# Performance work log

Measured on AMD Instinct MI355X. Metric: run time of the kernel, lower is better.

## Reference

```python
import jax, jax.numpy as jnp
import numpy as np
from jax import lax

B, P, T = 64, 16, 256
I, H, O = 256, 512, 5
V = 50000


def setup_inputs() -> dict:
    key = jax.random.key(0)
    ks = jax.random.split(key, 16)
    xav = lambda k, shape: jax.random.normal(k, shape, dtype=jnp.float32) * np.sqrt(2.0 / (shape[-2] + shape[-1]))
    inp = {
        "x": jax.random.randint(ks[0], (B, P, T), 0, V),
        "emb": jax.random.normal(ks[1], (V, I), dtype=jnp.float32) * 0.02,
        "W_forget_x": xav(ks[2], (P, I, H)),
        "W_forget_h": xav(ks[3], (H, H)),
        "b_forget": jnp.zeros((H,), jnp.float32),
        "W_ic_x": xav(ks[4], (P, I, H)),
        "W_ic_h": xav(ks[5], (H, H)),
        "b_ic": jnp.zeros((H,), jnp.float32),
        "W_in_x": xav(ks[6], (P, I, H)),
        "W_in_h": xav(ks[7], (H, H)),
        "b_in": jnp.zeros((H,), jnp.float32),
        "W_o_x": xav(ks[8], (P, I, H)),
        "W_o_h": xav(ks[9], (H, H)),
        "b_o": jnp.zeros((H,), jnp.float32),
        "W_lin": xav(ks[10], (H, O)),
        "b_lin": jnp.zeros((O,), jnp.float32),
    }
    return inp


def reference(x, emb, W_forget_x, W_forget_h, b_forget, W_ic_x, W_ic_h, b_ic,
              W_in_x, W_in_h, b_in, W_o_x, W_o_h, b_o, W_lin, b_lin):
    # padding_idx=0: row 0 of the embedding table is zero
    tbl = emb.at[0].set(0.0)
    xe = tbl[x]  # [B, P, T, I]
    # x-side gate pre-activations, summed over POS tags, hoisted out of the recurrence
    pre_f = jnp.einsum('bpti,pih->tbh', xe, W_forget_x) + b_forget  # [T, B, H]
    pre_i = jnp.einsum('bpti,pih->tbh', xe, W_ic_x) + b_ic
    pre_g = jnp.einsum('bpti,pih->tbh', xe, W_in_x) + b_in
    pre_o = jnp.einsum('bpti,pih->tbh', xe, W_o_x) + b_o

    def step(carry, pres):
        h, c = carry
        pf, pi, pg, po = pres
        f = jax.nn.sigmoid(pf + h @ W_forget_h)
        i = jax.nn.sigmoid(pi + h @ W_ic_h)
        g = jnp.tanh(pg + h @ W_in_h)
        o = jax.nn.sigmoid(po + h @ W_o_h)
        c = f * c + i * g
        h = o * jnp.tanh(c)
        return (h, c), None

    bs = x.shape[0]
    h0 = jnp.zeros((bs, W_forget_h.shape[0]), jnp.float32)
    c0 = jnp.zeros_like(h0)
    (h_t, c_t), _ = lax.scan(step, (h0, c0), (pre_f, pre_i, pre_g, pre_o))
    out = h_t @ W_lin + b_lin  # [B, O]
    return out, h_t, c_t
```

## Files before the change

### kernel.cpp

```cpp
#include <hip/hip_runtime.h>
#include <stdint.h>

#define DEVI __device__ __forceinline__
typedef unsigned long long ull;

typedef __bf16 bf16x8 __attribute__((ext_vector_type(8)));
typedef float floatx4 __attribute__((ext_vector_type(4)));

DEVI uint16_t f2bf(float f) {
  union { float f; uint32_t u; } c; c.f = f;
  uint32_t u = c.u;
  return (uint16_t)((u + 0x7fffu + ((u >> 16) & 1u)) >> 16);
}
DEVI float bf2f(uint16_t h) {
  union { uint32_t u; float f; } c; c.u = ((uint32_t)h) << 16;
  return c.f;
}
DEVI void load_lds_16(const void* g, void* l) {
  __builtin_amdgcn_global_load_lds(
      (const __attribute__((address_space(1))) void*)g,
      (__attribute__((address_space(3))) void*)l, 16, 0, 0);
}
DEVI float sigm(float x) { return 1.f / (1.f + __expf(-x)); }
DEVI float tanh_s(float x) {
  float xc = fminf(fmaxf(x, -15.f), 15.f);
  float e = __expf(2.f * xc);
  return (e - 1.f) / (e + 1.f);
}

static constexpr size_t OFF_EMB   = 0;
static constexpr size_t OFF_TS01  = 0;
static constexpr size_t OFF_WXT   = 25600000;
static constexpr size_t OFF_WHT   = OFF_WXT + 16777216;
static constexpr size_t OFF_BIAS  = OFF_WHT + 2097152;
static constexpr size_t OFF_PRE   = OFF_BIAS + 8192;
static constexpr size_t OFF_HF    = OFF_PRE + 67108864 + 4096;
static constexpr size_t OFF_CF    = OFF_HF + 131072;

__global__ __launch_bounds__(256) void k_emb_cvt(const float* __restrict__ emb,
                                                 uint16_t* __restrict__ dst) {
  size_t tid = (size_t)blockIdx.x * 256 + threadIdx.x;
  size_t e = tid * 8;
  int v = (int)(e >> 8);
  const float4* s = (const float4*)(emb + e);
  float4 f0 = s[0], f1 = s[1];
  if (v == 0) { f0 = make_float4(0.f, 0.f, 0.f, 0.f); f1 = f0; }
  uint32_t w0 = f2bf(f0.x) | ((uint32_t)f2bf(f0.y) << 16);
  uint32_t w1 = f2bf(f0.z) | ((uint32_t)f2bf(f0.w) << 16);
  uint32_t w2 = f2bf(f1.x) | ((uint32_t)f2bf(f1.y) << 16);
  uint32_t w3 = f2bf(f1.z) | ((uint32_t)f2bf(f1.w) << 16);
  *(uint4*)(dst + e) = make_uint4(w0, w1, w2, w3);
}

__global__ __launch_bounds__(256) void k_wt(const float* __restrict__ w0, const float* __restrict__ w1,
                                            const float* __restrict__ w2, const float* __restrict__ w3,
                                            int K, uint16_t* __restrict__ dst) {
  __shared__ float tile[64 * 64];
  int k0 = blockIdx.x * 64;
  int n0 = blockIdx.y * 64;
  int h0 = blockIdx.y * 16;
  int g = threadIdx.x >> 6, di = threadIdx.x & 63;
  const float* w = (g == 0) ? w0 : (g == 1) ? w1 : (g == 2) ? w2 : w3;
  const float4* src = (const float4*)(w + (size_t)(k0 + di) * 512 + h0);
  float4 a = src[0], b = src[1], c = src[2], d = src[3];
  float vals[16] = {a.x, a.y, a.z, a.w, b.x, b.y, b.z, b.w,
                    c.x, c.y, c.z, c.w, d.x, d.y, d.z, d.w};
#pragma unroll
  for (int dh = 0; dh < 16; ++dh) tile[(dh * 4 + g) * 64 + di] = vals[dh];
  __syncthreads();
  int nl = threadIdx.x >> 2, ch = threadIdx.x & 3;
  uint32_t wb[8];
#pragma unroll
  for (int j = 0; j < 8; ++j) {
    float lo = tile[nl * 64 + ch * 16 + j * 2];
    float hi = tile[nl * 64 + ch * 16 + j * 2 + 1];
    wb[j] = f2bf(lo) | ((uint32_t)f2bf(hi) << 16);
  }
  uint4* dp = (uint4*)(dst + (size_t)(n0 + nl) * K + k0 + ch * 16);
  dp[0] = make_uint4(wb[0], wb[1], wb[2], wb[3]);
  dp[1] = make_uint4(wb[4], wb[5], wb[6], wb[7]);
}

__global__ __launch_bounds__(256) void k_bias(const float* __restrict__ b0, const float* __restrict__ b1,
                                              const float* __restrict__ b2, const float* __restrict__ b3,
                                              float* __restrict__ dst) {
  int n = blockIdx.x * 256 + threadIdx.x;
  int h = n >> 2, g = n & 3;
  const float* b = (g == 0) ? b0 : (g == 1) ? b1 : (g == 2) ? b2 : b3;
  dst[n] = b[h];
}

__global__ __launch_bounds__(256) void k_gemm(const uint16_t* __restrict__ embbf,
                                              const int* __restrict__ x,
                                              const uint16_t* __restrict__ wxt,
                                              uint16_t* __restrict__ pre) {
  __shared__ uint16_t As[128 * 64];
  __shared__ uint16_t Bs[128 * 64];
  const int tid = threadIdx.x;
  const int wv = tid >> 6, ln = tid & 63;
  const int wm = wv >> 1, wn = wv & 1;
  const int M0 = blockIdx.x * 128, N0 = blockIdx.y * 128;
  const int srow = ln >> 3, schunk = ln & 7;

  const int* xrow[4];
  const uint16_t* bbase[4];
  uint16_t* ldsA[4];
  uint16_t* ldsB[4];
#pragma unroll
  for (int j = 0; j < 4; ++j) {
    int r = j * 32 + wv * 8 + srow;
    int m = M0 + r;
    int t = m >> 6, b = m & 63;
    xrow[j] = x + b * 4096 + t;
    bbase[j] = wxt + (size_t)(N0 + r) * 4096 + schunk * 8;
    ldsA[j] = As + (j * 32 + wv * 8) * 64;
    ldsB[j] = Bs + (j * 32 + wv * 8) * 64;
  }

  const int q = ln >> 4, l16 = ln & 15;
  int aoff[4], boff[4];
#pragma unroll
  for (int mt = 0; mt < 4; ++mt) aoff[mt] = (wm * 64 + mt * 16 + l16) * 64 + q * 8;
#pragma unroll
  for (int nt = 0; nt < 4; ++nt) boff[nt] = (wn * 64 + nt * 16 + l16) * 64 + q * 8;

  floatx4 acc[4][4] = {};

  for (int p = 0; p < 16; ++p) {
    const uint16_t* abase[4];
#pragma unroll
    for (int j = 0; j < 4; ++j) {
      int idx = xrow[j][p << 8];
      abase[j] = embbf + (size_t)idx * 256 + schunk * 8;
    }
#pragma unroll 1
    for (int ki = 0; ki < 4; ++ki) {
      __syncthreads();
#pragma unroll
      for (int j = 0; j < 4; ++j) load_lds_16(abase[j] + ki * 64, ldsA[j]);
#pragma unroll
      for (int j = 0; j < 4; ++j) load_lds_16(bbase[j] + p * 256 + ki * 64, ldsB[j]);
      __syncthreads();
#pragma unroll
      for (int kk = 0; kk < 2; ++kk) {
        bf16x8 a[4];
#pragma unroll
        for (int mt = 0; mt < 4; ++mt) a[mt] = *(const bf16x8*)(As + aoff[mt] + kk * 32);
#pragma unroll
        for (int nt = 0; nt < 4; ++nt) {
          bf16x8 bv = *(const bf16x8*)(Bs + boff[nt] + kk * 32);
#pragma unroll
          for (int mt = 0; mt < 4; ++mt)
            acc[mt][nt] = __builtin_amdgcn_mfma_f32_16x16x32_bf16(a[mt], bv, acc[mt][nt], 0, 0, 0);
        }
      }
    }
  }

#pragma unroll
  for (int mt = 0; mt < 4; ++mt) {
    int mg = M0 + wm * 64 + mt * 16 + q * 4;
#pragma unroll
    for (int nt = 0; nt < 4; ++nt) {
      int ng = N0 + wn * 64 + nt * 16 + l16;
#pragma unroll
      for (int r = 0; r < 4; ++r)
        pre[(size_t)(mg + r) * 2048 + ng] = f2bf(acc[mt][nt][r]);
    }
  }
}

__global__ __launch_bounds__(256) void k_rec(const uint16_t* pre,
                                             char* preb,
                                             char* scratch,
                                             const uint16_t* __restrict__ wht,
                                             const float* __restrict__ bias,
                                             float* __restrict__ hfin,
                                             float* __restrict__ cfin) {
  __shared__ uint16_t Ahs[2][16 * 544];
  __shared__ uint16_t pres[2][16 * 128];
  __shared__ float gates[16 * 132];

  const int tid = threadIdx.x;
  const int wv = tid >> 6, ln = tid & 63;
  const int q = ln >> 4, l16 = ln & 15;
  const int bg = blockIdx.x >> 4, cg = blockIdx.x & 15;
  const int N0 = cg * 128;

  bf16x8 Bfrag[16][2];
#pragma unroll
  for (int kc = 0; kc < 16; ++kc)
#pragma unroll
    for (int nt = 0; nt < 2; ++nt) {
      int n = N0 + wv * 32 + nt * 16 + l16;
      Bfrag[kc][nt] = *(const bf16x8*)(wht + (size_t)n * 512 + kc * 32 + q * 8);
    }
  float breg[2];
#pragma unroll
  for (int nt = 0; nt < 2; ++nt) breg[nt] = bias[N0 + wv * 32 + nt * 16 + l16];

  const int prow = wv * 4 + (ln >> 4);
  const int pj = ln & 15;
  const int erow = ln >> 2;
  const int es = ln & 3;
  float creg[2] = {0.f, 0.f};

  for (int i = tid; i < 4352; i += 256) ((uint32_t*)Ahs[0])[i] = 0;
  {
    const uint16_t* g = pre + (size_t)(bg * 16 + wv * 4 + (ln >> 4)) * 2048 + N0 + (ln & 15) * 8;
    load_lds_16(g, (uint16_t*)pres[0] + wv * 512);
  }

  for (int t = 0; t < 256; ++t) {
    if (t > 0) {
      const char* sb = (t - 1 < 2) ? scratch + (size_t)(t - 1) * 262144
                                   : preb + (size_t)(t - 3) * 262144;
      const ull* pp = (const ull*)(sb + (size_t)bg * 65536 + prow * 2048 + pj * 8);
      const uint32_t want = (uint32_t)t;
      ull v[16];
      bool ok = false;
      while (!ok) {
        ok = true;
#pragma unroll
        for (int j = 0; j < 16; ++j)
          v[j] = __hip_atomic_load(pp + j * 16, __ATOMIC_RELAXED, __HIP_MEMORY_SCOPE_AGENT);
#pragma unroll
        for (int j = 0; j < 16; ++j)
          ok = ok && ((uint32_t)(v[j] >> 32) == want);
        if (!ok) __builtin_amdgcn_s_sleep(1);
      }
      uint16_t* dr = Ahs[t & 1] + prow * 544;
#pragma unroll
      for (int j = 0; j < 16; ++j)
        *(uint32_t*)(dr + 2 * pj + 32 * j) = (uint32_t)v[j];
    }
    __syncthreads();

    const uint16_t* Ab = Ahs[t & 1];
    floatx4 a0[2] = {}, a1[2] = {};
#pragma unroll
    for (int kc = 0; kc < 8; ++kc) {
      bf16x8 a = *(const bf16x8*)(Ab + l16 * 544 + kc * 32 + q * 8);
#pragma unroll
      for (int nt = 0; nt < 2; ++nt)
        a0[nt] = __builtin_amdgcn_mfma_f32_16x16x32_bf16(a, Bfrag[kc][nt], a0[nt], 0, 0, 0);
    }
#pragma unroll
    for (int kc = 8; kc < 16; ++kc) {
      bf16x8 a = *(const bf16x8*)(Ab + l16 * 544 + kc * 32 + q * 8);
#pragma unroll
      for (int nt = 0; nt < 2; ++nt)
        a1[nt] = __builtin_amdgcn_mfma_f32_16x16x32_bf16(a, Bfrag[kc][nt], a1[nt], 0, 0, 0);
    }

    const uint16_t* pcur = (const uint16_t*)pres[t & 1];
#pragma unroll
    for (int nt = 0; nt < 2; ++nt) {
      int n_l = wv * 32 + nt * 16 + l16;
      floatx4 s = a0[nt] + a1[nt];
#pragma unroll
      for (int r = 0; r < 4; ++r) {
        int row = q * 4 + r;
        gates[row * 132 + n_l] = s[r] + breg[nt] + bf2f(pcur[row * 128 + n_l]);
      }
    }

    {
      float4 v0 = *(const float4*)(gates + erow * 132 + wv * 32 + es * 8);
      float4 v1 = *(const float4*)(gates + erow * 132 + wv * 32 + es * 8 + 4);
      float f0 = sigm(v0.x), i0 = sigm(v0.y), g0 = tanh_s(v0.z), o0 = sigm(v0.w);
      float f1 = sigm(v1.x), i1 = sigm(v1.y), g1 = tanh_s(v1.z), o1 = sigm(v1.w);
      float c0 = f0 * creg[0] + i0 * g0; creg[0] = c0;
      float c1 = f1 * creg[1] + i1 * g1; creg[1] = c1;
      float h0 = o0 * tanh_s(c0), h1 = o1 * tanh_s(c1);
      char* sbw = (t < 2) ? scratch + (size_t)t * 262144
                          : preb + (size_t)(t - 2) * 262144;
      int pair = cg * 16 + wv * 4 + es;
      ull pk = (ull)((uint32_t)f2bf(h0) | ((uint32_t)f2bf(h1) << 16)) |
               ((ull)(uint32_t)(t + 1) << 32);
      __hip_atomic_store((ull*)(sbw + (size_t)bg * 65536 + erow * 2048 + pair * 8),
                         pk, __ATOMIC_RELAXED, __HIP_MEMORY_SCOPE_AGENT);
      if (t == 255) {
        size_t idx = (size_t)(bg * 16 + erow) * 512 + cg * 32 + wv * 8 + es * 2;
        hfin[idx] = h0; hfin[idx + 1] = h1;
        cfin[idx] = c0; cfin[idx + 1] = c1;
      }
    }

    {
      int tn = (t < 255) ? t + 1 : 255;
      const uint16_t* g = pre + (size_t)(tn * 64 + bg * 16 + wv * 4 + (ln >> 4)) * 2048 + N0 + (ln & 15) * 8;
      load_lds_16(g, (uint16_t*)pres[(t + 1) & 1] + wv * 512);
    }
  }
}

__global__ __launch_bounds__(256) void k_final(const float* __restrict__ h, const float* __restrict__ c,
                                               const float* __restrict__ wl, const float* __restrict__ bl,
                                               float* __restrict__ out) {
  __shared__ float red[256];
  int b = blockIdx.x, t = threadIdx.x;
  const float* hb = h + (size_t)b * 512;
  if (t < 128) {
    ((float4*)(out + 320 + (size_t)b * 512))[t] = ((const float4*)hb)[t];
    ((float4*)(out + 320 + 32768 + (size_t)b * 512))[t] = ((const float4*)(c + (size_t)b * 512))[t];
  }
  float h0 = hb[t], h1 = hb[t + 256];
  for (int o = 0; o < 5; ++o) {
    red[t] = h0 * wl[t * 5 + o] + h1 * wl[(t + 256) * 5 + o];
    __syncthreads();
    for (int s = 128; s > 0; s >>= 1) {
      if (t < s) red[t] += red[t + s];
      __syncthreads();
    }
    if (t == 0) out[b * 5 + o] = red[0] + bl[o];
    __syncthreads();
  }
}

extern "C" void kernel_launch(void* const* d_in, const int* in_sizes, int n_in,
                              void* d_out, int out_size, void* d_ws, size_t ws_size,
                              hipStream_t stream) {
  const int*   x   = (const int*)d_in[0];
  const float* emb = (const float*)d_in[1];
  const float* wfx = (const float*)d_in[2];
  const float* wfh = (const float*)d_in[3];
  const float* bf_ = (const float*)d_in[4];
  const float* wix = (const float*)d_in[5];
  const float* wih = (const float*)d_in[6];
  const float* bi_ = (const float*)d_in[7];
  const float* wgx = (const float*)d_in[8];
  const float* wgh = (const float*)d_in[9];
  const float* bg_ = (const float*)d_in[10];
  const float* wox = (const float*)d_in[11];
  const float* woh = (const float*)d_in[12];
  const float* bo_ = (const float*)d_in[13];
  const float* wl  = (const float*)d_in[14];
  const float* bl  = (const float*)d_in[15];
  float* out = (float*)d_out;
  char* ws = (char*)d_ws;

  uint16_t* embbf = (uint16_t*)(ws + OFF_EMB);
  uint16_t* wxt   = (uint16_t*)(ws + OFF_WXT);
  uint16_t* wht   = (uint16_t*)(ws + OFF_WHT);
  float*    bias  = (float*)(ws + OFF_BIAS);
  uint16_t* pre   = (uint16_t*)(ws + OFF_PRE);
  float*    hfin  = (float*)(ws + OFF_HF);
  float*    cfin  = (float*)(ws + OFF_CF);

  hipLaunchKernelGGL(k_emb_cvt, dim3(6250), dim3(256), 0, stream, emb, embbf);
  hipLaunchKernelGGL(k_wt, dim3(64, 32), dim3(256), 0, stream, wfx, wix, wgx, wox, 4096, wxt);
  hipLaunchKernelGGL(k_wt, dim3(8, 32), dim3(256), 0, stream, wfh, wih, wgh, woh, 512, wht);
  hipLaunchKernelGGL(k_bias, dim3(8), dim3(256), 0, stream, bf_, bi_, bg_, bo_, bias);
  hipLaunchKernelGGL(k_gemm, dim3(128, 16), dim3(256), 0, stream, embbf, x, wxt, pre);
  hipLaunchKernelGGL(k_rec, dim3(64), dim3(256), 0, stream, pre, (char*)(ws + OFF_PRE),
                     ws + OFF_TS01, wht, bias, hfin, cfin);
  hipLaunchKernelGGL(k_final, dim3(64), dim3(256), 0, stream, hfin, cfin, wl, bl, out);
}
```

Baseline: 1.142 ms.

## Fuse input GEMM and LSTM recurrence into one kernel with per-tile readiness counters

```diff
diff --git a/kernel.cpp b/kernel.cpp
--- a/kernel.cpp
+++ b/kernel.cpp
@@ -28,14 +28,15 @@
   return (e - 1.f) / (e + 1.f);
 }
 
-static constexpr size_t OFF_EMB   = 0;
-static constexpr size_t OFF_TS01  = 0;
-static constexpr size_t OFF_WXT   = 25600000;
-static constexpr size_t OFF_WHT   = OFF_WXT + 16777216;
-static constexpr size_t OFF_BIAS  = OFF_WHT + 2097152;
-static constexpr size_t OFF_PRE   = OFF_BIAS + 8192;
-static constexpr size_t OFF_HF    = OFF_PRE + 67108864 + 4096;
-static constexpr size_t OFF_CF    = OFF_HF + 131072;
+static constexpr size_t OFF_EMB    = 0;
+static constexpr size_t OFF_WXT    = 25600000;
+static constexpr size_t OFF_WHT    = OFF_WXT + 16777216;
+static constexpr size_t OFF_BIAS   = OFF_WHT + 2097152;
+static constexpr size_t OFF_PRE    = OFF_BIAS + 8192;
+static constexpr size_t OFF_HF     = OFF_PRE + 67108864 + 4096;
+static constexpr size_t OFF_CF     = OFF_HF + 131072;
+static constexpr size_t OFF_CNT    = OFF_CF + 131072;
+static constexpr size_t OFF_SLAB01 = OFF_CNT + 4096;
 
 __global__ __launch_bounds__(256) void k_emb_cvt(const float* __restrict__ emb,
                                                  uint16_t* __restrict__ dst) {
@@ -90,100 +91,98 @@
   dst[n] = b[h];
 }
 
-__global__ __launch_bounds__(256) void k_gemm(const uint16_t* __restrict__ embbf,
-                                              const int* __restrict__ x,
-                                              const uint16_t* __restrict__ wxt,
-                                              uint16_t* __restrict__ pre) {
-  __shared__ uint16_t As[128 * 64];
-  __shared__ uint16_t Bs[128 * 64];
-  const int tid = threadIdx.x;
-  const int wv = tid >> 6, ln = tid & 63;
-  const int wm = wv >> 1, wn = wv & 1;
-  const int M0 = blockIdx.x * 128, N0 = blockIdx.y * 128;
-  const int srow = ln >> 3, schunk = ln & 7;
-
-  const int* xrow[4];
-  const uint16_t* bbase[4];
-  uint16_t* ldsA[4];
-  uint16_t* ldsB[4];
-#pragma unroll
-  for (int j = 0; j < 4; ++j) {
-    int r = j * 32 + wv * 8 + srow;
-    int m = M0 + r;
-    int t = m >> 6, b = m & 63;
-    xrow[j] = x + b * 4096 + t;
-    bbase[j] = wxt + (size_t)(N0 + r) * 4096 + schunk * 8;
-    ldsA[j] = As + (j * 32 + wv * 8) * 64;
-    ldsB[j] = Bs + (j * 32 + wv * 8) * 64;
-  }
-
-  const int q = ln >> 4, l16 = ln & 15;
-  int aoff[4], boff[4];
-#pragma unroll
-  for (int mt = 0; mt < 4; ++mt) aoff[mt] = (wm * 64 + mt * 16 + l16) * 64 + q * 8;
-#pragma unroll
-  for (int nt = 0; nt < 4; ++nt) boff[nt] = (wn * 64 + nt * 16 + l16) * 64 + q * 8;
-
-  floatx4 acc[4][4] = {};
-
-  for (int p = 0; p < 16; ++p) {
-    const uint16_t* abase[4];
-#pragma unroll
-    for (int j = 0; j < 4; ++j) {
-      int idx = xrow[j][p << 8];
-      abase[j] = embbf + (size_t)idx * 256 + schunk * 8;
-    }
-#pragma unroll 1
-    for (int ki = 0; ki < 4; ++ki) {
-      __syncthreads();
-#pragma unroll
-      for (int j = 0; j < 4; ++j) load_lds_16(abase[j] + ki * 64, ldsA[j]);
-#pragma unroll
-      for (int j = 0; j < 4; ++j) load_lds_16(bbase[j] + p * 256 + ki * 64, ldsB[j]);
-      __syncthreads();
-#pragma unroll
-      for (int kk = 0; kk < 2; ++kk) {
-        bf16x8 a[4];
-#pragma unroll
-        for (int mt = 0; mt < 4; ++mt) a[mt] = *(const bf16x8*)(As + aoff[mt] + kk * 32);
-#pragma unroll
-        for (int nt = 0; nt < 4; ++nt) {
-          bf16x8 bv = *(const bf16x8*)(Bs + boff[nt] + kk * 32);
-#pragma unroll
-          for (int mt = 0; mt < 4; ++mt)
-            acc[mt][nt] = __builtin_amdgcn_mfma_f32_16x16x32_bf16(a[mt], bv, acc[mt][nt], 0, 0, 0);
-        }
-      }
-    }
-  }
-
-#pragma unroll
-  for (int mt = 0; mt < 4; ++mt) {
-    int mg = M0 + wm * 64 + mt * 16 + q * 4;
-#pragma unroll
-    for (int nt = 0; nt < 4; ++nt) {
-      int ng = N0 + wn * 64 + nt * 16 + l16;
-#pragma unroll
-      for (int r = 0; r < 4; ++r)
-        pre[(size_t)(mg + r) * 2048 + ng] = f2bf(acc[mt][nt][r]);
-    }
-  }
-}
-
-__global__ __launch_bounds__(256) void k_rec(const uint16_t* pre,
-                                             char* preb,
-                                             char* scratch,
-                                             const uint16_t* __restrict__ wht,
-                                             const float* __restrict__ bias,
-                                             float* __restrict__ hfin,
-                                             float* __restrict__ cfin) {
-  __shared__ uint16_t Ahs[2][16 * 544];
-  __shared__ uint16_t pres[2][16 * 128];
-  __shared__ float gates[16 * 132];
-
+__global__ __launch_bounds__(256) void k_main(const uint16_t* embbf, const int* x,
+                                              const uint16_t* wxt, uint16_t* pre,
+                                              char* preb, char* slab01,
+                                              const uint16_t* wht, const float* biasp,
+                                              int* cnt, float* hfin, float* cfin) {
+  __shared__ __align__(16) char smem[43264];
   const int tid = threadIdx.x;
   const int wv = tid >> 6, ln = tid & 63;
   const int q = ln >> 4, l16 = ln & 15;
+
+  if (blockIdx.x >= 64) {
+    const int bid = blockIdx.x - 64;
+    const int mtile = bid >> 4;
+    const int M0 = mtile * 128, N0 = (bid & 15) * 128;
+    uint16_t* As = (uint16_t*)smem;
+    uint16_t* Bs = As + 128 * 64;
+    const int wm = wv >> 1, wn = wv & 1;
+    const int srow = ln >> 3, schunk = ln & 7;
+
+    const int* xrow[4];
+    const uint16_t* bbase[4];
+    uint16_t* ldsA[4];
+    uint16_t* ldsB[4];
+#pragma unroll
+    for (int j = 0; j < 4; ++j) {
+      int r = j * 32 + wv * 8 + srow;
+      int m = M0 + r;
+      int t = m >> 6, b = m & 63;
+      xrow[j] = x + b * 4096 + t;
+      bbase[j] = wxt + (size_t)(N0 + r) * 4096 + schunk * 8;
+      ldsA[j] = As + (j * 32 + wv * 8) * 64;
+      ldsB[j] = Bs + (j * 32 + wv * 8) * 64;
+    }
+    int aoff[4], boff[4];
+#pragma unroll
+    for (int mt = 0; mt < 4; ++mt) aoff[mt] = (wm * 64 + mt * 16 + l16) * 64 + q * 8;
+#pragma unroll
+    for (int nt = 0; nt < 4; ++nt) boff[nt] = (wn * 64 + nt * 16 + l16) * 64 + q * 8;
+
+    floatx4 acc[4][4] = {};
+    for (int p = 0; p < 16; ++p) {
+      const uint16_t* abase[4];
+#pragma unroll
+      for (int j = 0; j < 4; ++j) {
+        int idx = xrow[j][p << 8];
+        abase[j] = embbf + (size_t)idx * 256 + schunk * 8;
+      }
+#pragma unroll 1
+      for (int ki = 0; ki < 4; ++ki) {
+        __syncthreads();
+#pragma unroll
+        for (int j = 0; j < 4; ++j) load_lds_16(abase[j] + ki * 64, ldsA[j]);
+#pragma unroll
+        for (int j = 0; j < 4; ++j) load_lds_16(bbase[j] + p * 256 + ki * 64, ldsB[j]);
+        __syncthreads();
+#pragma unroll
+        for (int kk = 0; kk < 2; ++kk) {
+          bf16x8 a[4];
+#pragma unroll
+          for (int mt = 0; mt < 4; ++mt) a[mt] = *(const bf16x8*)(As + aoff[mt] + kk * 32);
+#pragma unroll
+          for (int nt = 0; nt < 4; ++nt) {
+            bf16x8 bv = *(const bf16x8*)(Bs + boff[nt] + kk * 32);
+#pragma unroll
+            for (int mt = 0; mt < 4; ++mt)
+              acc[mt][nt] = __builtin_amdgcn_mfma_f32_16x16x32_bf16(a[mt], bv, acc[mt][nt], 0, 0, 0);
+          }
+        }
+      }
+    }
+#pragma unroll
+    for (int mt = 0; mt < 4; ++mt) {
+      int mg = M0 + wm * 64 + mt * 16 + q * 4;
+#pragma unroll
+      for (int nt = 0; nt < 4; ++nt) {
+        int ng = N0 + wn * 64 + nt * 16 + l16;
+#pragma unroll
+        for (int r = 0; r < 4; ++r)
+          pre[(size_t)(mg + r) * 2048 + ng] = f2bf(acc[mt][nt][r]);
+      }
+    }
+    __syncthreads();
+    if (tid == 0)
+      __hip_atomic_fetch_add(&cnt[mtile], 1, __ATOMIC_RELEASE, __HIP_MEMORY_SCOPE_AGENT);
+    return;
+  }
+
+  uint16_t* Ahs[2];
+  Ahs[0] = (uint16_t*)smem;
+  Ahs[1] = Ahs[0] + 16 * 544;
+  float* gates = (float*)(smem + 34816);
+
   const int bg = blockIdx.x >> 4, cg = blockIdx.x & 15;
   const int N0 = cg * 128;
 
@@ -197,7 +196,7 @@
     }
   float breg[2];
 #pragma unroll
-  for (int nt = 0; nt < 2; ++nt) breg[nt] = bias[N0 + wv * 32 + nt * 16 + l16];
+  for (int nt = 0; nt < 2; ++nt) breg[nt] = biasp[N0 + wv * 32 + nt * 16 + l16];
 
   const int prow = wv * 4 + (ln >> 4);
   const int pj = ln & 15;
@@ -206,14 +205,28 @@
   float creg[2] = {0.f, 0.f};
 
   for (int i = tid; i < 4352; i += 256) ((uint32_t*)Ahs[0])[i] = 0;
-  {
-    const uint16_t* g = pre + (size_t)(bg * 16 + wv * 4 + (ln >> 4)) * 2048 + N0 + (ln & 15) * 8;
-    load_lds_16(g, (uint16_t*)pres[0] + wv * 512);
-  }
+
+  int done_m = -1;
+  auto wait_mtile = [&](int m) {
+    if (m > done_m) {
+      while (__hip_atomic_load(&cnt[m], __ATOMIC_RELAXED, __HIP_MEMORY_SCOPE_AGENT) < 16)
+        __builtin_amdgcn_s_sleep(8);
+      __builtin_amdgcn_fence(__ATOMIC_ACQUIRE, "agent");
+      done_m = m;
+    }
+  };
+
+  uint16_t pr[8];
+  wait_mtile(0);
+#pragma unroll
+  for (int nt = 0; nt < 2; ++nt)
+#pragma unroll
+    for (int r = 0; r < 4; ++r)
+      pr[nt * 4 + r] = pre[(size_t)(bg * 16 + q * 4 + r) * 2048 + N0 + wv * 32 + nt * 16 + l16];
 
   for (int t = 0; t < 256; ++t) {
     if (t > 0) {
-      const char* sb = (t - 1 < 2) ? scratch + (size_t)(t - 1) * 262144
+      const char* sb = (t - 1 < 2) ? slab01 + (size_t)(t - 1) * 262144
                                    : preb + (size_t)(t - 3) * 262144;
       const ull* pp = (const ull*)(sb + (size_t)bg * 65536 + prow * 2048 + pj * 8);
       const uint32_t want = (uint32_t)t;
@@ -253,7 +266,6 @@
         a1[nt] = __builtin_amdgcn_mfma_f32_16x16x32_bf16(a, Bfrag[kc][nt], a1[nt], 0, 0, 0);
     }
 
-    const uint16_t* pcur = (const uint16_t*)pres[t & 1];
 #pragma unroll
     for (int nt = 0; nt < 2; ++nt) {
       int n_l = wv * 32 + nt * 16 + l16;
@@ -261,7 +273,7 @@
 #pragma unroll
       for (int r = 0; r < 4; ++r) {
         int row = q * 4 + r;
-        gates[row * 132 + n_l] = s[r] + breg[nt] + bf2f(pcur[row * 128 + n_l]);
+        gates[row * 132 + n_l] = s[r] + breg[nt] + bf2f(pr[nt * 4 + r]);
       }
     }
 
@@ -273,7 +285,7 @@
       float c0 = f0 * creg[0] + i0 * g0; creg[0] = c0;
       float c1 = f1 * creg[1] + i1 * g1; creg[1] = c1;
       float h0 = o0 * tanh_s(c0), h1 = o1 * tanh_s(c1);
-      char* sbw = (t < 2) ? scratch + (size_t)t * 262144
+      char* sbw = (t < 2) ? slab01 + (size_t)t * 262144
                           : preb + (size_t)(t - 2) * 262144;
       int pair = cg * 16 + wv * 4 + es;
       ull pk = (ull)((uint32_t)f2bf(h0) | ((uint32_t)f2bf(h1) << 16)) |
@@ -287,10 +299,14 @@
       }
     }
 
-    {
-      int tn = (t < 255) ? t + 1 : 255;
-      const uint16_t* g = pre + (size_t)(tn * 64 + bg * 16 + wv * 4 + (ln >> 4)) * 2048 + N0 + (ln & 15) * 8;
-      load_lds_16(g, (uint16_t*)pres[(t + 1) & 1] + wv * 512);
+    if (t < 255) {
+      int tn = t + 1;
+      wait_mtile(tn >> 1);
+#pragma unroll
+      for (int nt = 0; nt < 2; ++nt)
+#pragma unroll
+        for (int r = 0; r < 4; ++r)
+          pr[nt * 4 + r] = pre[(size_t)(tn * 64 + bg * 16 + q * 4 + r) * 2048 + N0 + wv * 32 + nt * 16 + l16];
     }
   }
 }
@@ -347,13 +363,16 @@
   uint16_t* pre   = (uint16_t*)(ws + OFF_PRE);
   float*    hfin  = (float*)(ws + OFF_HF);
   float*    cfin  = (float*)(ws + OFF_CF);
+  int*      cnt   = (int*)(ws + OFF_CNT);
+
+  hipMemsetAsync(ws + OFF_CNT, 0, 4096, stream);
 
   hipLaunchKernelGGL(k_emb_cvt, dim3(6250), dim3(256), 0, stream, emb, embbf);
   hipLaunchKernelGGL(k_wt, dim3(64, 32), dim3(256), 0, stream, wfx, wix, wgx, wox, 4096, wxt);
   hipLaunchKernelGGL(k_wt, dim3(8, 32), dim3(256), 0, stream, wfh, wih, wgh, woh, 512, wht);
   hipLaunchKernelGGL(k_bias, dim3(8), dim3(256), 0, stream, bf_, bi_, bg_, bo_, bias);
-  hipLaunchKernelGGL(k_gemm, dim3(128, 16), dim3(256), 0, stream, embbf, x, wxt, pre);
-  hipLaunchKernelGGL(k_rec, dim3(64), dim3(256), 0, stream, pre, (char*)(ws + OFF_PRE),
-                     ws + OFF_TS01, wht, bias, hfin, cfin);
+  hipLaunchKernelGGL(k_main, dim3(64 + 2048), dim3(256), 0, stream,
+                     embbf, x, wxt, pre, (char*)(ws + OFF_PRE), ws + OFF_SLAB01,
+                     wht, bias, cnt, hfin, cfin);
   hipLaunchKernelGGL(k_final, dim3(64), dim3(256), 0, stream, hfin, cfin, wl, bl, out);
 }
```

Result: slower. 1.285 ms (+12.5%).

## Widen recurrence polling loads and keep pre-activations in registers

Applied to the files above, without the earlier changes.

```diff
diff --git a/kernel.cpp b/kernel.cpp
--- a/kernel.cpp
+++ b/kernel.cpp
@@ -6,6 +6,7 @@
 
 typedef __bf16 bf16x8 __attribute__((ext_vector_type(8)));
 typedef float floatx4 __attribute__((ext_vector_type(4)));
+typedef unsigned int u32x4 __attribute__((ext_vector_type(4)));
 
 DEVI uint16_t f2bf(float f) {
   union { float f; uint32_t u; } c; c.f = f;
@@ -28,14 +29,15 @@
   return (e - 1.f) / (e + 1.f);
 }
 
-static constexpr size_t OFF_EMB   = 0;
-static constexpr size_t OFF_TS01  = 0;
-static constexpr size_t OFF_WXT   = 25600000;
-static constexpr size_t OFF_WHT   = OFF_WXT + 16777216;
-static constexpr size_t OFF_BIAS  = OFF_WHT + 2097152;
-static constexpr size_t OFF_PRE   = OFF_BIAS + 8192;
-static constexpr size_t OFF_HF    = OFF_PRE + 67108864 + 4096;
-static constexpr size_t OFF_CF    = OFF_HF + 131072;
+static constexpr size_t OFF_EMB    = 0;
+static constexpr size_t OFF_WXT    = 25600000;
+static constexpr size_t OFF_WHT    = OFF_WXT + 16777216;
+static constexpr size_t OFF_BIAS   = OFF_WHT + 2097152;
+static constexpr size_t OFF_PRE    = OFF_BIAS + 8192;
+static constexpr size_t OFF_HF     = OFF_PRE + 67108864 + 4096;
+static constexpr size_t OFF_CF     = OFF_HF + 131072;
+static constexpr size_t OFF_CNT    = OFF_CF + 131072;
+static constexpr size_t OFF_SLAB01 = OFF_CNT + 4096;
 
 __global__ __launch_bounds__(256) void k_emb_cvt(const float* __restrict__ emb,
                                                  uint16_t* __restrict__ dst) {
@@ -174,11 +176,10 @@
                                              char* preb,
                                              char* scratch,
                                              const uint16_t* __restrict__ wht,
-                                             const float* __restrict__ bias,
+                                             const float* __restrict__ biasp,
                                              float* __restrict__ hfin,
                                              float* __restrict__ cfin) {
-  __shared__ uint16_t Ahs[2][16 * 544];
-  __shared__ uint16_t pres[2][16 * 128];
+  __shared__ uint16_t Ahs[2][16 * 528];
   __shared__ float gates[16 * 132];
 
   const int tid = threadIdx.x;
@@ -197,42 +198,61 @@
     }
   float breg[2];
 #pragma unroll
-  for (int nt = 0; nt < 2; ++nt) breg[nt] = bias[N0 + wv * 32 + nt * 16 + l16];
-
-  const int prow = wv * 4 + (ln >> 4);
-  const int pj = ln & 15;
+  for (int nt = 0; nt < 2; ++nt) breg[nt] = biasp[N0 + wv * 32 + nt * 16 + l16];
+
+  const int prow = tid >> 4;
+  const int pseg = tid & 15;
   const int erow = ln >> 2;
   const int es = ln & 3;
   float creg[2] = {0.f, 0.f};
 
-  for (int i = tid; i < 4352; i += 256) ((uint32_t*)Ahs[0])[i] = 0;
-  {
-    const uint16_t* g = pre + (size_t)(bg * 16 + wv * 4 + (ln >> 4)) * 2048 + N0 + (ln & 15) * 8;
-    load_lds_16(g, (uint16_t*)pres[0] + wv * 512);
-  }
+  for (int i = tid; i < 4224; i += 256) ((uint32_t*)Ahs[0])[i] = 0;
+
+  uint16_t pr[8];
+#pragma unroll
+  for (int nt = 0; nt < 2; ++nt)
+#pragma unroll
+    for (int r = 0; r < 4; ++r)
+      pr[nt * 4 + r] = pre[(size_t)(bg * 16 + q * 4 + r) * 2048 + N0 + wv * 32 + nt * 16 + l16];
 
   for (int t = 0; t < 256; ++t) {
     if (t > 0) {
-      const char* sb = (t - 1 < 2) ? scratch + (size_t)(t - 1) * 262144
-                                   : preb + (size_t)(t - 3) * 262144;
-      const ull* pp = (const ull*)(sb + (size_t)bg * 65536 + prow * 2048 + pj * 8);
+      const char* sb = ((t - 1) < 2 ? scratch + (size_t)(t - 1) * 262144
+                                    : preb + (size_t)(t - 3) * 262144) + (size_t)bg * 65536;
+      const char* base = sb + prow * 2048 + pseg * 16;
       const uint32_t want = (uint32_t)t;
-      ull v[16];
-      bool ok = false;
-      while (!ok) {
-        ok = true;
-#pragma unroll
-        for (int j = 0; j < 16; ++j)
-          v[j] = __hip_atomic_load(pp + j * 16, __ATOMIC_RELAXED, __HIP_MEMORY_SCOPE_AGENT);
-#pragma unroll
-        for (int j = 0; j < 16; ++j)
-          ok = ok && ((uint32_t)(v[j] >> 32) == want);
-        if (!ok) __builtin_amdgcn_s_sleep(1);
+      u32x4 u0, u1, u2, u3, u4, u5, u6, u7;
+      for (;;) {
+        asm volatile(
+            "global_load_dwordx4 %0, %8, off sc0 sc1\n\t"
+            "global_load_dwordx4 %1, %8, off offset:256 sc0 sc1\n\t"
+            "global_load_dwordx4 %2, %8, off offset:512 sc0 sc1\n\t"
+            "global_load_dwordx4 %3, %8, off offset:768 sc0 sc1\n\t"
+            "global_load_dwordx4 %4, %8, off offset:1024 sc0 sc1\n\t"
+            "global_load_dwordx4 %5, %8, off offset:1280 sc0 sc1\n\t"
+            "global_load_dwordx4 %6, %8, off offset:1536 sc0 sc1\n\t"
+            "global_load_dwordx4 %7, %8, off offset:1792 sc0 sc1\n\t"
+            "s_waitcnt vmcnt(0)"
+            : "=v"(u0), "=v"(u1), "=v"(u2), "=v"(u3),
+              "=v"(u4), "=v"(u5), "=v"(u6), "=v"(u7)
+            : "v"(base)
+            : "memory");
+        bool ok = (u0.y == want) && (u0.w == want) && (u1.y == want) && (u1.w == want) &&
+                  (u2.y == want) && (u2.w == want) && (u3.y == want) && (u3.w == want) &&
+                  (u4.y == want) && (u4.w == want) && (u5.y == want) && (u5.w == want) &&
+                  (u6.y == want) && (u6.w == want) && (u7.y == want) && (u7.w == want);
+        if (ok) break;
+        __builtin_amdgcn_s_sleep(1);
       }
-      uint16_t* dr = Ahs[t & 1] + prow * 544;
-#pragma unroll
-      for (int j = 0; j < 16; ++j)
-        *(uint32_t*)(dr + 2 * pj + 32 * j) = (uint32_t)v[j];
+      uint16_t* dr = Ahs[t & 1] + prow * 528 + pseg * 4;
+      *(ull*)(dr +   0) = (ull)u0.x | ((ull)u0.z << 32);
+      *(ull*)(dr +  64) = (ull)u1.x | ((ull)u1.z << 32);
+      *(ull*)(dr + 128) = (ull)u2.x | ((ull)u2.z << 32);
+      *(ull*)(dr + 192) = (ull)u3.x | ((ull)u3.z << 32);
+      *(ull*)(dr + 256) = (ull)u4.x | ((ull)u4.z << 32);
+      *(ull*)(dr + 320) = (ull)u5.x | ((ull)u5.z << 32);
+      *(ull*)(dr + 384) = (ull)u6.x | ((ull)u6.z << 32);
+      *(ull*)(dr + 448) = (ull)u7.x | ((ull)u7.z << 32);
     }
     __syncthreads();
 
@@ -240,20 +260,19 @@
     floatx4 a0[2] = {}, a1[2] = {};
 #pragma unroll
     for (int kc = 0; kc < 8; ++kc) {
-      bf16x8 a = *(const bf16x8*)(Ab + l16 * 544 + kc * 32 + q * 8);
+      bf16x8 a = *(const bf16x8*)(Ab + l16 * 528 + kc * 32 + q * 8);
 #pragma unroll
       for (int nt = 0; nt < 2; ++nt)
         a0[nt] = __builtin_amdgcn_mfma_f32_16x16x32_bf16(a, Bfrag[kc][nt], a0[nt], 0, 0, 0);
     }
 #pragma unroll
     for (int kc = 8; kc < 16; ++kc) {
-      bf16x8 a = *(const bf16x8*)(Ab + l16 * 544 + kc * 32 + q * 8);
+      bf16x8 a = *(const bf16x8*)(Ab + l16 * 528 + kc * 32 + q * 8);
 #pragma unroll
       for (int nt = 0; nt < 2; ++nt)
         a1[nt] = __builtin_amdgcn_mfma_f32_16x16x32_bf16(a, Bfrag[kc][nt], a1[nt], 0, 0, 0);
     }
 
-    const uint16_t* pcur = (const uint16_t*)pres[t & 1];
 #pragma unroll
     for (int nt = 0; nt < 2; ++nt) {
       int n_l = wv * 32 + nt * 16 + l16;
@@ -261,7 +280,7 @@
 #pragma unroll
       for (int r = 0; r < 4; ++r) {
         int row = q * 4 + r;
-        gates[row * 132 + n_l] = s[r] + breg[nt] + bf2f(pcur[row * 128 + n_l]);
+        gates[row * 132 + n_l] = s[r] + breg[nt] + bf2f(pr[nt * 4 + r]);
       }
     }
 
@@ -273,12 +292,12 @@
       float c0 = f0 * creg[0] + i0 * g0; creg[0] = c0;
       float c1 = f1 * creg[1] + i1 * g1; creg[1] = c1;
       float h0 = o0 * tanh_s(c0), h1 = o1 * tanh_s(c1);
-      char* sbw = (t < 2) ? scratch + (size_t)t * 262144
-                          : preb + (size_t)(t - 2) * 262144;
+      char* sbw = (t < 2 ? scratch + (size_t)t * 262144
+                         : preb + (size_t)(t - 2) * 262144) + (size_t)bg * 65536;
       int pair = cg * 16 + wv * 4 + es;
       ull pk = (ull)((uint32_t)f2bf(h0) | ((uint32_t)f2bf(h1) << 16)) |
                ((ull)(uint32_t)(t + 1) << 32);
-      __hip_atomic_store((ull*)(sbw + (size_t)bg * 65536 + erow * 2048 + pair * 8),
+      __hip_atomic_store((ull*)(sbw + erow * 2048 + pair * 8),
                          pk, __ATOMIC_RELAXED, __HIP_MEMORY_SCOPE_AGENT);
       if (t == 255) {
         size_t idx = (size_t)(bg * 16 + erow) * 512 + cg * 32 + wv * 8 + es * 2;
@@ -287,10 +306,13 @@
       }
     }
 
-    {
-      int tn = (t < 255) ? t + 1 : 255;
-      const uint16_t* g = pre + (size_t)(tn * 64 + bg * 16 + wv * 4 + (ln >> 4)) * 2048 + N0 + (ln & 15) * 8;
-      load_lds_16(g, (uint16_t*)pres[(t + 1) & 1] + wv * 512);
+    if (t < 255) {
+      int tn = t + 1;
+#pragma unroll
+      for (int nt = 0; nt < 2; ++nt)
+#pragma unroll
+        for (int r = 0; r < 4; ++r)
+          pr[nt * 4 + r] = pre[(size_t)(tn * 64 + bg * 16 + q * 4 + r) * 2048 + N0 + wv * 32 + nt * 16 + l16];
     }
   }
 }
@@ -354,6 +376,6 @@
   hipLaunchKernelGGL(k_bias, dim3(8), dim3(256), 0, stream, bf_, bi_, bg_, bo_, bias);
   hipLaunchKernelGGL(k_gemm, dim3(128, 16), dim3(256), 0, stream, embbf, x, wxt, pre);
   hipLaunchKernelGGL(k_rec, dim3(64), dim3(256), 0, stream, pre, (char*)(ws + OFF_PRE),
-                     ws + OFF_TS01, wht, bias, hfin, cfin);
+                     ws + OFF_SLAB01, wht, bias, hfin, cfin);
   hipLaunchKernelGGL(k_final, dim3(64), dim3(256), 0, stream, hfin, cfin, wl, bl, out);
 }
```

After: 1.021 ms. -10.6%, faster.
